# Optimization experiments

Hardware: AMD Instinct MI355X
Metric: run time of the kernel (lower is better)

## Reference

```python
import jax, jax.numpy as jnp
import numpy as np

LR = 0.01            # learning_rate
PC = 0.001           # pred_clipping
WC = 5.0             # weight_clipping
_LO = float(np.log(PC / (1.0 - PC)))   # logit(pred_clipping)
_HI = -_LO                              # logit(1 - pred_clipping)


def setup_inputs() -> dict:
    B, S, I, CTX, M, C = 64, 1023, 1024, 784, 4, 1  # S = size-1 (bias row), C = num_classes->1
    key = jax.random.key(0)
    k = jax.random.split(key, 6)
    logit = jax.random.normal(k[0], (B, I, C), jnp.float32)
    context = jax.random.normal(k[1], (B, CTX), jnp.float32)
    target = jax.random.uniform(k[2], (B, C), dtype=jnp.float32)
    cm = jax.random.normal(k[3], (C, S, M, CTX), jnp.float32)
    cm = cm / jnp.linalg.norm(cm, axis=-1, keepdims=True)          # unit-norm context maps
    cb = jax.random.normal(k[4], (C, S, M, 1), jnp.float32)        # context bias
    weights = jnp.full((C, S, 2 ** M, I), 1.0 / I, jnp.float32)    # per-context weight table
    bias = jax.random.uniform(k[5], (1, 1, C), jnp.float32, _LO, _HI)
    return {"logit": logit, "context": context, "target": target,
            "context_maps": cm, "context_bias": cb, "weights": weights, "bias": bias}


def reference(logit, context, target, context_maps, context_bias, weights, bias):
    C, S, M, _ = context_maps.shape
    B = context.shape[0]
    # halfspace hashing of the context -> per-(class, neuron, sample) weight-table index
    dist = jnp.einsum('csmk,bk->csmb', context_maps, context)      # [C,S,M,B]
    bits = (dist > context_bias).astype(jnp.int32)
    conv = (2 ** jnp.arange(M, dtype=jnp.int32))[:, None]          # [M,1]
    idx = jnp.sum(bits * conv, axis=-2)                            # [C,S,B] in [0, 2^M)
    ci = jnp.arange(C)[:, None, None]
    si = jnp.arange(S)[None, :, None]
    sel = weights[ci, si, idx]                                     # gather -> [C,S,B,I]
    # batched dot product (torch code does full matmul + diagonal; this is the same math)
    out = jnp.clip(jnp.einsum('csbi,bic->csb', sel, logit), _LO, _HI)
    out_bsc = out.transpose(2, 1, 0)                               # [B,S,C]
    # online weight update (target branch): gather-compute-scatter
    diff = jax.nn.sigmoid(out_bsc) - target[:, None, :]            # [B,S,C]
    upd = LR * diff[..., None] * logit.transpose(0, 2, 1)[:, None, :, :]  # [B,S,C,I]
    new_sel = jnp.clip(sel - upd.transpose(2, 1, 0, 3), -WC, WC)   # [C,S,B,I]
    new_weights = weights.at[ci, si, idx].set(new_sel)             # scatter
    # prepend constant bias neuron
    out_logits = jnp.concatenate([jnp.broadcast_to(bias, (B, 1, C)), out_bsc], axis=1)  # [B,S+1,C]
    return out_logits, new_weights
```

## Files before the change

kernel.cpp:

```cpp
#include <hip/hip_runtime.h>
#include <math.h>

typedef unsigned long long u64;
typedef __attribute__((ext_vector_type(8))) short bf16x8;
typedef __attribute__((ext_vector_type(4))) float f32x4;

#define S_DIM 1023
#define B_DIM 64
#define I_DIM 1024
#define CTX_DIM 784
#define CTX4 196
#define NWROWS 16
#define NTASK (S_DIM * NWROWS)

#define LR_C 0.01f
#define WC_C 5.0f
#define LO_C (-6.906754778648554f)
#define HI_C ( 6.906754778648554f)

__device__ __forceinline__ float dot4(float4 a, float4 b) {
    return a.x * b.x + a.y * b.y + a.z * b.z + a.w * b.w;
}

__device__ __forceinline__ float4 upd4(float4 w, float4 a, float c) {
    float4 r;
    r.x = fminf(fmaxf(w.x - c * a.x, -WC_C), WC_C);
    r.y = fminf(fmaxf(w.y - c * a.y, -WC_C), WC_C);
    r.z = fminf(fmaxf(w.z - c * a.z, -WC_C), WC_C);
    r.w = fminf(fmaxf(w.w - c * a.w, -WC_C), WC_C);
    return r;
}

__device__ __forceinline__ short f2bf(float f) {
    union { float f; unsigned u; } cv; cv.f = f;
    unsigned r = cv.u + 0x7fffu + ((cv.u >> 16) & 1u);
    return (short)(r >> 16);
}

__global__ __launch_bounds__(256) void prep_kernel(
    const float* __restrict__ context,
    const float* __restrict__ bias,
    float4* __restrict__ ctxT4,
    float* __restrict__ out_logits)
{
    int g = blockIdx.x * 256 + threadIdx.x;
    int k4 = g >> 6;
    int b  = g & 63;
    ctxT4[g] = *(const float4*)(context + (size_t)b * CTX_DIM + k4 * 4);
    if (g < B_DIM) out_logits[(size_t)g * (S_DIM + 1)] = bias[0];
}

__global__ __launch_bounds__(256) void pack_kernel(
    const float* __restrict__ logit,
    short* __restrict__ pack_b)
{
    int g = blockIdx.x * 256 + threadIdx.x;
    int l  = g & 63;
    int kb = (g >> 6) & 31;
    int nt = g >> 11;
    int b  = nt * 16 + (l & 15);
    int i0 = kb * 32 + (l >> 4) * 8;
    const float* src = logit + (size_t)b * I_DIM + i0;
    bf16x8 v;
    #pragma unroll
    for (int j = 0; j < 8; ++j) v[j] = f2bf(src[j]);
    *(bf16x8*)(pack_b + (size_t)g * 8) = v;
}

__global__ __launch_bounds__(256) void gln_idx_kernel(
    const float* __restrict__ cm,
    const float* __restrict__ cb,
    const float4* __restrict__ ctxT4,
    u64* __restrict__ mask_g)
{
    __shared__ float red[4][4][64];
    __shared__ int   bits[4][64];
    __shared__ float cb_lds[4];

    const int s = blockIdx.x;
    const int t = threadIdx.x;
    if (t < 4) cb_lds[t] = cb[s * 4 + t];

    const int b = t & 63;
    const int q = __builtin_amdgcn_readfirstlane(t >> 6);
    const float4* cmr = (const float4*)(cm + (size_t)s * 4 * CTX_DIM);

    float a0 = 0.f, a1 = 0.f, a2 = 0.f, a3 = 0.f;
    const int k0 = q * 49;
    #pragma unroll 7
    for (int kk = 0; kk < 49; ++kk) {
        int k4 = k0 + kk;
        float4 c4 = ctxT4[k4 * 64 + b];
        a0 += dot4(cmr[k4], c4);
        a1 += dot4(cmr[CTX4 + k4], c4);
        a2 += dot4(cmr[2 * CTX4 + k4], c4);
        a3 += dot4(cmr[3 * CTX4 + k4], c4);
    }
    red[q][0][b] = a0;
    red[q][1][b] = a1;
    red[q][2][b] = a2;
    red[q][3][b] = a3;
    __syncthreads();

    {
        int m = t >> 6, bb = t & 63;
        float sum = red[0][m][bb] + red[1][m][bb] + red[2][m][bb] + red[3][m][bb];
        bits[m][bb] = (sum > cb_lds[m]) ? 1 : 0;
    }
    __syncthreads();

    if (t < B_DIM) {
        int v = bits[0][t] + 2 * bits[1][t] + 4 * bits[2][t] + 8 * bits[3][t];
        u64 my = 0;
        #pragma unroll
        for (int kk = 0; kk < NWROWS; ++kk) {
            u64 mk = __ballot(v == kk);
            if (t == kk) my = mk;
        }
        if (t < NWROWS) mask_g[s * NWROWS + t] = my;
    }
}

__global__ __launch_bounds__(256, 4) void gln_mfma2_kernel(
    const float* __restrict__ logit,
    const float* __restrict__ target,
    const float* __restrict__ weights,
    const u64*   __restrict__ mask_g,
    const short* __restrict__ pack_b,
    float* __restrict__ out_logits,
    float* __restrict__ new_weights)
{
    __shared__ short Abf[NWROWS * I_DIM];
    __shared__ u64   mask_lds[NWROWS];
    __shared__ int   lastb_lds[NWROWS];
    __shared__ float coef_lds[NWROWS];

    const int s  = blockIdx.x;
    const int t  = threadIdx.x;
    const int wv = t >> 6;
    const int l  = t & 63;

    if (t < NWROWS) {
        u64 m = mask_g[s * NWROWS + t];
        mask_lds[t]  = m;
        lastb_lds[t] = m ? (63 - __clzll(m)) : -1;
    }

    const float4* W4 = (const float4*)(weights + (size_t)s * (NWROWS * I_DIM));
    #pragma unroll
    for (int j = 0; j < 16; ++j) {
        float4 w = W4[t + j * 256];
        int slot = j * 128 + (((t >> 1)) ^ (j & 7));
        short4 v;
        v.x = f2bf(w.x); v.y = f2bf(w.y); v.z = f2bf(w.z); v.w = f2bf(w.w);
        *(short4*)(Abf + slot * 8 + (t & 1) * 4) = v;
    }
    __syncthreads();

    const int row = l & 15;
    const int q   = l >> 4;
    const int sw  = row & 7;
    const int base_slot = row * 128;
    const bf16x8* Bb = (const bf16x8*)pack_b + (size_t)wv * 2048 + l;
    f32x4 acc = {0.f, 0.f, 0.f, 0.f};
    #pragma unroll 8
    for (int kb = 0; kb < 32; ++kb) {
        bf16x8 af = *(const bf16x8*)(Abf + 8 * (base_slot + ((kb * 4 + q) ^ sw)));
        bf16x8 bfr = Bb[(size_t)kb * 64];
        acc = __builtin_amdgcn_mfma_f32_16x16x32_bf16(af, bfr, acc, 0, 0, 0);
    }

    const int col = wv * 16 + (l & 15);
    #pragma unroll
    for (int j = 0; j < 4; ++j) {
        int r = q * 4 + j;
        u64 m = mask_lds[r];
        if ((m >> col) & 1) {
            float o = fminf(fmaxf(acc[j], LO_C), HI_C);
            out_logits[(size_t)col * (S_DIM + 1) + s + 1] = o;
            if (col == lastb_lds[r])
                coef_lds[r] = LR_C * (1.0f / (1.0f + expf(-o)) - target[col]);
        }
    }
    __syncthreads();

    float4*       D4 = (float4*)(new_weights + (size_t)s * (NWROWS * I_DIM));
    const float4* L4 = (const float4*)logit;
    #pragma unroll 8
    for (int r = 0; r < NWROWS; ++r) {
        const int lb = lastb_lds[r];
        float4 w = W4[r * 256 + t];
        float4 o;
        if (lb < 0) {
            o = w;
        } else {
            o = upd4(w, L4[lb * 256 + t], coef_lds[r]);
        }
        D4[r * 256 + t] = o;
    }
}

extern "C" void kernel_launch(void* const* d_in, const int* in_sizes, int n_in,
                              void* d_out, int out_size, void* d_ws, size_t ws_size,
                              hipStream_t stream) {
    const float* logit   = (const float*)d_in[0];
    const float* context = (const float*)d_in[1];
    const float* target  = (const float*)d_in[2];
    const float* cm      = (const float*)d_in[3];
    const float* cb      = (const float*)d_in[4];
    const float* weights = (const float*)d_in[5];
    const float* bias    = (const float*)d_in[6];

    float* out_logits  = (float*)d_out;
    float* new_weights = out_logits + (size_t)B_DIM * (S_DIM + 1);

    char* ws = (char*)d_ws;
    float4* ctxT4  = (float4*)ws;    ws += (size_t)CTX4 * B_DIM * 16;
    u64*    mask_g = (u64*)ws;       ws += (size_t)NTASK * 8;
    short*  packb  = (short*)ws;

    prep_kernel<<<CTX4 * B_DIM / 256, 256, 0, stream>>>(context, bias, ctxT4, out_logits);
    pack_kernel<<<32, 256, 0, stream>>>(logit, packb);
    gln_idx_kernel<<<S_DIM, 256, 0, stream>>>(cm, cb, ctxT4, mask_g);
    gln_mfma2_kernel<<<S_DIM, 256, 0, stream>>>(logit, target, weights, mask_g, packb,
                                                out_logits, new_weights);
}
```

Measured before the change: 63.89 us.

## Fuse context hashing into MFMA kernel and keep weight tile in registers

Merges the halfspace-hash index kernel into the main MFMA/update kernel, so the per-row masks stay in shared memory instead of going through a global buffer, and one kernel launch is removed. The block's 16x1024 weight slice is loaded once into registers at the start. Those registers are reused for both the bf16 LDS staging and the final clipped update, which avoids a second global read of the weights. The weight loads are issued early, so their latency overlaps the context dot products. The cost is heavy register pressure (16 float4 per thread) under launch bounds of 4 blocks, which may cause spills or lower occupancy.

New measurement: 58.81 us. -7.9%, faster.

```diff
diff --git a/kernel.cpp b/kernel.cpp
--- a/kernel.cpp
+++ b/kernel.cpp
@@ -11,7 +11,6 @@
 #define CTX_DIM 784
 #define CTX4 196
 #define NWROWS 16
-#define NTASK (S_DIM * NWROWS)
 
 #define LR_C 0.01f
 #define WC_C 5.0f
@@ -67,48 +66,64 @@
     *(bf16x8*)(pack_b + (size_t)g * 8) = v;
 }
 
-__global__ __launch_bounds__(256) void gln_idx_kernel(
+__global__ __launch_bounds__(256, 4) void gln_fused_kernel(
+    const float* __restrict__ logit,
+    const float* __restrict__ target,
+    const float* __restrict__ weights,
     const float* __restrict__ cm,
     const float* __restrict__ cb,
     const float4* __restrict__ ctxT4,
-    u64* __restrict__ mask_g)
+    const short* __restrict__ pack_b,
+    float* __restrict__ out_logits,
+    float* __restrict__ new_weights)
 {
+    __shared__ short Abf[NWROWS * I_DIM];
     __shared__ float red[4][4][64];
     __shared__ int   bits[4][64];
     __shared__ float cb_lds[4];
-
-    const int s = blockIdx.x;
-    const int t = threadIdx.x;
+    __shared__ u64   mask_lds[NWROWS];
+    __shared__ int   lastb_lds[NWROWS];
+    __shared__ float coef_lds[NWROWS];
+
+    const int s  = blockIdx.x;
+    const int t  = threadIdx.x;
+    const int wv = t >> 6;
+    const int l  = t & 63;
+
+    const float4* W4 = (const float4*)(weights + (size_t)s * (NWROWS * I_DIM));
+    float4 Wr[16];
+    #pragma unroll
+    for (int j = 0; j < 16; ++j) Wr[j] = W4[t + j * 256];
+
     if (t < 4) cb_lds[t] = cb[s * 4 + t];
 
-    const int b = t & 63;
-    const int q = __builtin_amdgcn_readfirstlane(t >> 6);
-    const float4* cmr = (const float4*)(cm + (size_t)s * 4 * CTX_DIM);
-
-    float a0 = 0.f, a1 = 0.f, a2 = 0.f, a3 = 0.f;
-    const int k0 = q * 49;
-    #pragma unroll 7
-    for (int kk = 0; kk < 49; ++kk) {
-        int k4 = k0 + kk;
-        float4 c4 = ctxT4[k4 * 64 + b];
-        a0 += dot4(cmr[k4], c4);
-        a1 += dot4(cmr[CTX4 + k4], c4);
-        a2 += dot4(cmr[2 * CTX4 + k4], c4);
-        a3 += dot4(cmr[3 * CTX4 + k4], c4);
-    }
-    red[q][0][b] = a0;
-    red[q][1][b] = a1;
-    red[q][2][b] = a2;
-    red[q][3][b] = a3;
-    __syncthreads();
-
+    {
+        const int b = t & 63;
+        const int q = __builtin_amdgcn_readfirstlane(t >> 6);
+        const float4* cmr = (const float4*)(cm + (size_t)s * 4 * CTX_DIM);
+        float a0 = 0.f, a1 = 0.f, a2 = 0.f, a3 = 0.f;
+        const int k0 = q * 49;
+        #pragma unroll 7
+        for (int kk = 0; kk < 49; ++kk) {
+            int k4 = k0 + kk;
+            float4 c4 = ctxT4[k4 * 64 + b];
+            a0 += dot4(cmr[k4], c4);
+            a1 += dot4(cmr[CTX4 + k4], c4);
+            a2 += dot4(cmr[2 * CTX4 + k4], c4);
+            a3 += dot4(cmr[3 * CTX4 + k4], c4);
+        }
+        red[q][0][b] = a0;
+        red[q][1][b] = a1;
+        red[q][2][b] = a2;
+        red[q][3][b] = a3;
+    }
+    __syncthreads();
     {
         int m = t >> 6, bb = t & 63;
         float sum = red[0][m][bb] + red[1][m][bb] + red[2][m][bb] + red[3][m][bb];
         bits[m][bb] = (sum > cb_lds[m]) ? 1 : 0;
     }
     __syncthreads();
-
     if (t < B_DIM) {
         int v = bits[0][t] + 2 * bits[1][t] + 4 * bits[2][t] + 8 * bits[3][t];
         u64 my = 0;
@@ -117,55 +132,31 @@
             u64 mk = __ballot(v == kk);
             if (t == kk) my = mk;
         }
-        if (t < NWROWS) mask_g[s * NWROWS + t] = my;
-    }
-}
-
-__global__ __launch_bounds__(256, 4) void gln_mfma2_kernel(
-    const float* __restrict__ logit,
-    const float* __restrict__ target,
-    const float* __restrict__ weights,
-    const u64*   __restrict__ mask_g,
-    const short* __restrict__ pack_b,
-    float* __restrict__ out_logits,
-    float* __restrict__ new_weights)
-{
-    __shared__ short Abf[NWROWS * I_DIM];
-    __shared__ u64   mask_lds[NWROWS];
-    __shared__ int   lastb_lds[NWROWS];
-    __shared__ float coef_lds[NWROWS];
-
-    const int s  = blockIdx.x;
-    const int t  = threadIdx.x;
-    const int wv = t >> 6;
-    const int l  = t & 63;
-
-    if (t < NWROWS) {
-        u64 m = mask_g[s * NWROWS + t];
-        mask_lds[t]  = m;
-        lastb_lds[t] = m ? (63 - __clzll(m)) : -1;
-    }
-
-    const float4* W4 = (const float4*)(weights + (size_t)s * (NWROWS * I_DIM));
+        if (t < NWROWS) {
+            mask_lds[t]  = my;
+            lastb_lds[t] = my ? (63 - __clzll(my)) : -1;
+        }
+    }
+
     #pragma unroll
     for (int j = 0; j < 16; ++j) {
-        float4 w = W4[t + j * 256];
-        int slot = j * 128 + (((t >> 1)) ^ (j & 7));
+        int slot = j * 128 + ((t >> 1) ^ (j & 7));
         short4 v;
-        v.x = f2bf(w.x); v.y = f2bf(w.y); v.z = f2bf(w.z); v.w = f2bf(w.w);
+        v.x = f2bf(Wr[j].x); v.y = f2bf(Wr[j].y);
+        v.z = f2bf(Wr[j].z); v.w = f2bf(Wr[j].w);
         *(short4*)(Abf + slot * 8 + (t & 1) * 4) = v;
     }
     __syncthreads();
 
     const int row = l & 15;
-    const int q   = l >> 4;
+    const int q2  = l >> 4;
     const int sw  = row & 7;
     const int base_slot = row * 128;
     const bf16x8* Bb = (const bf16x8*)pack_b + (size_t)wv * 2048 + l;
     f32x4 acc = {0.f, 0.f, 0.f, 0.f};
     #pragma unroll 8
     for (int kb = 0; kb < 32; ++kb) {
-        bf16x8 af = *(const bf16x8*)(Abf + 8 * (base_slot + ((kb * 4 + q) ^ sw)));
+        bf16x8 af = *(const bf16x8*)(Abf + 8 * (base_slot + ((kb * 4 + q2) ^ sw)));
         bf16x8 bfr = Bb[(size_t)kb * 64];
         acc = __builtin_amdgcn_mfma_f32_16x16x32_bf16(af, bfr, acc, 0, 0, 0);
     }
@@ -173,7 +164,7 @@
     const int col = wv * 16 + (l & 15);
     #pragma unroll
     for (int j = 0; j < 4; ++j) {
-        int r = q * 4 + j;
+        int r = q2 * 4 + j;
         u64 m = mask_lds[r];
         if ((m >> col) & 1) {
             float o = fminf(fmaxf(acc[j], LO_C), HI_C);
@@ -186,15 +177,14 @@
 
     float4*       D4 = (float4*)(new_weights + (size_t)s * (NWROWS * I_DIM));
     const float4* L4 = (const float4*)logit;
-    #pragma unroll 8
+    #pragma unroll
     for (int r = 0; r < NWROWS; ++r) {
         const int lb = lastb_lds[r];
-        float4 w = W4[r * 256 + t];
         float4 o;
         if (lb < 0) {
-            o = w;
+            o = Wr[r];
         } else {
-            o = upd4(w, L4[lb * 256 + t], coef_lds[r]);
+            o = upd4(Wr[r], L4[lb * 256 + t], coef_lds[r]);
         }
         D4[r * 256 + t] = o;
     }
@@ -215,13 +205,11 @@
     float* new_weights = out_logits + (size_t)B_DIM * (S_DIM + 1);
 
     char* ws = (char*)d_ws;
-    float4* ctxT4  = (float4*)ws;    ws += (size_t)CTX4 * B_DIM * 16;
-    u64*    mask_g = (u64*)ws;       ws += (size_t)NTASK * 8;
-    short*  packb  = (short*)ws;
+    float4* ctxT4 = (float4*)ws;     ws += (size_t)CTX4 * B_DIM * 16;
+    short*  packb = (short*)ws;
 
     prep_kernel<<<CTX4 * B_DIM / 256, 256, 0, stream>>>(context, bias, ctxT4, out_logits);
     pack_kernel<<<32, 256, 0, stream>>>(logit, packb);
-    gln_idx_kernel<<<S_DIM, 256, 0, stream>>>(cm, cb, ctxT4, mask_g);
-    gln_mfma2_kernel<<<S_DIM, 256, 0, stream>>>(logit, target, weights, mask_g, packb,
-                                                out_logits, new_weights);
-}
+    gln_fused_kernel<<<S_DIM, 256, 0, stream>>>(logit, target, weights, cm, cb,
+                                                ctxT4, packb, out_logits, new_weights);
+}
```
